# Kernel optimization log

Measured on AMD Instinct MI355X. Metric: run time of the kernel, lower is better.

The kernel has to match this reference:

```python
import jax, jax.numpy as jnp
import numpy as np

STRIDE, PAD, DIL = 1, 1, 1  # from init_kwargs
RELU = True


def setup_inputs() -> dict:
    key = jax.random.key(0)
    k1, k2, k3 = jax.random.split(key, 3)
    B, Cin, Cout, H, W, K = 32, 128, 256, 56, 56, 3
    # uint8 quantized codes stored as float32 (module does .float() before conv)
    x = jnp.round(jax.random.uniform(k1, (B, Cin, H, W), dtype=jnp.float32) * 255.0)
    weight = jnp.round(jax.random.uniform(k2, (Cout, Cin, K, K), dtype=jnp.float32) * 255.0)
    # int32 quantized bias (scale = s_x * s_w, zero_point = 0)
    bias = jnp.round(jax.random.normal(k3, (Cout,), dtype=jnp.float32) * 1000.0)
    return {
        "x": x,
        "weight": weight,
        "bias": bias,
        "M": jnp.float32(0.0021),      # s_x * s_w / s_y
        "x_zero": jnp.float32(128.0),
        "w_zero": jnp.float32(127.0),
        "y_zero": jnp.float32(0.0),
    }


def reference(x, weight, bias, M, x_zero, w_zero, y_zero):
    # x: [B, Cin, H, W] uint8 codes as float; weight: [Cout, Cin, kh, kw]
    xz = x - x_zero                    # zero-point sub (padding adds literal 0s, as in torch: pad AFTER sub)
    w = weight - w_zero
    y = jax.lax.conv_general_dilated(
        xz, w,
        window_strides=(STRIDE, STRIDE),
        padding=((PAD, PAD), (PAD, PAD)),
        rhs_dilation=(DIL, DIL),
        dimension_numbers=("NCHW", "OIHW", "NCHW"),
    )
    y = (y + bias[None, :, None, None]) * M + y_zero  # requantize
    if RELU:
        y = jnp.maximum(y, y_zero)     # clamp below at output zero-point
    return jnp.round(y)
```

## Files before the change

### kernel.cpp

```cpp
#include <hip/hip_runtime.h>
#include <hip/hip_bf16.h>


typedef __attribute__((ext_vector_type(4))) int   i32x4;
typedef __attribute__((ext_vector_type(4))) float f32x4;

#define WTI8_BYTES (18 * 16384)
#define XPI8_BYTES (32 * 58 * 8192)

__device__ __forceinline__ void gload_lds16(const void* g, void* l) {
    __builtin_amdgcn_global_load_lds(
        (const __attribute__((address_space(1))) void*)g,
        (__attribute__((address_space(3))) void*)l, 16, 0, 0);
}

__global__ void wprep_kernel(const float* __restrict__ w, char* __restrict__ wt) {
    int cidx = blockIdx.x * 256 + threadIdx.x;
    int byte0 = cidx * 16;
    int s    = byte0 >> 14;
    int wn   = (byte0 >> 12) & 3;
    int e4   = byte0 & 4095;
    int nn   = e4 >> 6;
    int koff = e4 & 63;
    int kl   = koff ^ ((nn & 3) << 4);
    int n = wn * 64 + nn;
    int r = s >> 1, ch = s & 1;
    union { char c[16]; i32x4 v; } u;
#pragma unroll
    for (int j = 0; j < 16; ++j) {
        int cin = ch * 64 + kl + j;
        u.c[j] = (char)((int)w[(size_t)n * 1152 + cin * 9 + r] - 128);
    }
    *(i32x4*)(wt + byte0) = u.v;
}

__global__ void xprep_kernel(const float* __restrict__ x, const float* __restrict__ xzp,
                             char* __restrict__ xpi8, int* __restrict__ colsum) {
    int bhh = blockIdx.x;
    int b = bhh / 58, hh = bhh % 58;
    int tid = threadIdx.x;
    char* blob = xpi8 + (size_t)bhh * 8192;
    int w  = tid & 63;
    int cq = tid >> 6;
    __shared__ int ps[4][64];
    if (hh == 0 || hh == 57) {
        i32x4 z = {0, 0, 0, 0};
        *(i32x4*)(blob + tid * 32)      = z;
        *(i32x4*)(blob + tid * 32 + 16) = z;
        if (cq == 0) colsum[bhh * 64 + w] = 0;
        return;
    }
    const int ZX = (int)rintf(*xzp);
    bool valid = (w >= 1 && w <= 56);
    const float* xb = x + (size_t)b * 128 * 3136 + (size_t)(hh - 1) * 56 +
                      (valid ? (w - 1) : 0);
    int csum = 0;
#pragma unroll
    for (int u = 0; u < 2; ++u) {
        union { char c[16]; i32x4 v; } uu;
#pragma unroll
        for (int j = 0; j < 16; ++j) {
            int c = cq * 32 + u * 16 + j;
            int val = valid ? ((int)xb[(size_t)c * 3136] - ZX) : 0;
            uu.c[j] = (char)val;
            csum += val;
        }
        *(i32x4*)(blob + w * 128 + ((cq * 32 + u * 16) ^ ((w & 7) << 4))) = uu.v;
    }
    ps[cq][w] = csum;
    __syncthreads();
    if (cq == 0)
        colsum[bhh * 64 + w] = ps[0][w] + ps[1][w] + ps[2][w] + ps[3][w];
}

__global__ __launch_bounds__(256, 2)
void conv_kernel(const char* __restrict__ wt,
                 const char* __restrict__ xpi8,
                 const int* __restrict__ colsum,
                 const float* __restrict__ bias,
                 const float* __restrict__ Mp,
                 const float* __restrict__ wzp,
                 const float* __restrict__ yzp,
                 float* __restrict__ out) {
    __shared__ __align__(1024) char As[32768];
    __shared__ __align__(1024) char Bp[32768];
    __shared__ int s2row[2][64];

    const int tid = threadIdx.x;
    const int lane = tid & 63;
    const int wn = tid >> 6;
    const int l15 = lane & 15, lg = lane >> 4;
    const int bx = blockIdx.x;
    const int b = bx / 28;
    const int h0 = (bx % 28) * 2;

    char* bpriv = Bp + wn * 8192;
    const char* bwsrc = wt + wn * 4096 + lane * 16;
    const int bfoff = (lg * 16) ^ ((l15 & 3) << 4);

    const char* agbase = xpi8 + (size_t)(b * 58 + h0) * 8192;
#pragma unroll
    for (int i = 0; i < 8; ++i)
        gload_lds16(agbase + i * 4096 + tid * 16, As + i * 4096 + tid * 16);
#pragma unroll
    for (int st = 0; st < 2; ++st)
#pragma unroll
        for (int i = 0; i < 4; ++i)
            gload_lds16(bwsrc + (size_t)st * 16384 + i * 1024,
                        bpriv + st * 4096 + i * 1024 + lane * 16);
    if (tid < 128) {
        int row = tid >> 6, m = tid & 63;
        int s = 0;
        if (m < 56) {
#pragma unroll
            for (int kh = 0; kh < 3; ++kh)
#pragma unroll
                for (int kw = 0; kw < 3; ++kw)
                    s += colsum[(b * 58 + h0 + row + kh) * 64 + m + kw];
        }
        s2row[row][m] = s;
    }

    i32x4 acc[4][8];
#pragma unroll
    for (int i = 0; i < 4; ++i)
#pragma unroll
        for (int j = 0; j < 8; ++j)
            acc[i][j] = (i32x4){0, 0, 0, 0};

    __syncthreads();

#pragma unroll
    for (int s = 0; s < 18; ++s) {
        const int kh = (s >> 1) / 3, kw = (s >> 1) % 3, ch = s & 1;
        const char* bslot = bpriv + (s & 1) * 4096;
        i32x4 bfr[4];
#pragma unroll
        for (int fn = 0; fn < 4; ++fn) {
            int nn = fn * 16 + l15;
            bfr[fn] = *(const i32x4*)(bslot + nn * 64 + bfoff);
        }
        i32x4 afr[8];
#pragma unroll
        for (int fm = 0; fm < 8; ++fm) {
            int rowoff = fm >> 2;
            int wv = (fm & 3) * 16 + l15 + kw;
            int wc = wv > 63 ? 63 : wv;
            int ab = (rowoff + kh) * 8192 + wc * 128 +
                     ((ch * 64 + lg * 16) ^ ((wc & 7) << 4));
            afr[fm] = *(const i32x4*)(As + ab);
        }
        if (s < 16) {
            asm volatile("s_waitcnt lgkmcnt(0)" ::: "memory");
#pragma unroll
            for (int i = 0; i < 4; ++i)
                gload_lds16(bwsrc + (size_t)(s + 2) * 16384 + i * 1024,
                            bpriv + (s & 1) * 4096 + i * 1024 + lane * 16);
        }
        if (s < 16)       asm volatile("s_waitcnt vmcnt(4)" ::: "memory");
        else if (s == 16) asm volatile("s_waitcnt vmcnt(0)" ::: "memory");
#pragma unroll
        for (int fn = 0; fn < 4; ++fn)
#pragma unroll
            for (int fm = 0; fm < 8; ++fm)
                acc[fn][fm] = __builtin_amdgcn_mfma_i32_16x16x64_i8(
                    bfr[fn], afr[fm], acc[fn][fm], 0, 0, 0);
    }

    const float Mv  = *Mp;
    const float yzv = *yzp;
    const float CWf = 128.0f - *wzp;
#pragma unroll
    for (int fn = 0; fn < 4; ++fn) {
#pragma unroll
        for (int reg = 0; reg < 4; ++reg) {
            const int cout = wn * 64 + fn * 16 + lg * 4 + reg;
            const float bv = bias[cout];
#pragma unroll
            for (int fm = 0; fm < 8; ++fm) {
                const int row = fm >> 2;
                const int m = (fm & 3) * 16 + l15;
                if (m < 56) {
                    const size_t rowb =
                        ((size_t)(b * 256 + cout) * 56 + h0 + row) * 56;
                    float af = (float)acc[fn][fm][reg] +
                               CWf * (float)s2row[row][m];
                    float v = (af + bv) * Mv + yzv;
                    v = fmaxf(v, yzv);
                    out[rowb + m] = rintf(v);
                }
            }
        }
    }
}

extern "C" void kernel_launch(void* const* d_in, const int* in_sizes, int n_in,
                              void* d_out, int out_size, void* d_ws, size_t ws_size,
                              hipStream_t stream) {
    const float* x    = (const float*)d_in[0];
    const float* w    = (const float*)d_in[1];
    const float* bias = (const float*)d_in[2];
    const float* Mp   = (const float*)d_in[3];
    const float* xzp  = (const float*)d_in[4];
    const float* wzp  = (const float*)d_in[5];
    const float* yzp  = (const float*)d_in[6];
    float* out = (float*)d_out;

    char* wt     = (char*)d_ws;
    char* xpi8   = wt + WTI8_BYTES;
    int*  colsum = (int*)(xpi8 + XPI8_BYTES);

    wprep_kernel<<<72, 256, 0, stream>>>(w, wt);
    xprep_kernel<<<32 * 58, 256, 0, stream>>>(x, xzp, xpi8, colsum);
    conv_kernel<<<32 * 28, 256, 0, stream>>>(wt, xpi8, colsum, bias, Mp, wzp, yzp, out);
}
```

Before: 75.46 us.

## Stage conv epilogue through LDS for vector stores and merge prep kernels

The epilogue now writes requantized outputs into a shared-memory buffer per output row, then stores them to global memory as 16-byte vectors, replacing scattered scalar stores. The weight and activation prep kernels are merged into one launch to save a kernel launch and the gap between launches. The shared allocation grows to about 68 KB, which with the launch bound of 2 blocks per CU may limit occupancy, and the epilogue adds block barriers.

After: 75.20 us. No clear change (-0.3%).

```diff
diff --git a/kernel.cpp b/kernel.cpp
--- a/kernel.cpp
+++ b/kernel.cpp
@@ -14,46 +14,48 @@
         (__attribute__((address_space(3))) void*)l, 16, 0, 0);
 }
 
-__global__ void wprep_kernel(const float* __restrict__ w, char* __restrict__ wt) {
-    int cidx = blockIdx.x * 256 + threadIdx.x;
-    int byte0 = cidx * 16;
-    int s    = byte0 >> 14;
-    int wn   = (byte0 >> 12) & 3;
-    int e4   = byte0 & 4095;
-    int nn   = e4 >> 6;
-    int koff = e4 & 63;
-    int kl   = koff ^ ((nn & 3) << 4);
-    int n = wn * 64 + nn;
-    int r = s >> 1, ch = s & 1;
-    union { char c[16]; i32x4 v; } u;
-#pragma unroll
-    for (int j = 0; j < 16; ++j) {
-        int cin = ch * 64 + kl + j;
-        u.c[j] = (char)((int)w[(size_t)n * 1152 + cin * 9 + r] - 128);
-    }
-    *(i32x4*)(wt + byte0) = u.v;
-}
-
-__global__ void xprep_kernel(const float* __restrict__ x, const float* __restrict__ xzp,
-                             char* __restrict__ xpi8, int* __restrict__ colsum) {
+__global__ void prep_kernel(const float* __restrict__ x, const float* __restrict__ xzp,
+                            const float* __restrict__ w,
+                            char* __restrict__ xpi8, int* __restrict__ colsum,
+                            char* __restrict__ wt) {
+    int tid = threadIdx.x;
+    if (blockIdx.x >= 32 * 58) {
+        int cidx = (blockIdx.x - 32 * 58) * 256 + tid;
+        int byte0 = cidx * 16;
+        int s    = byte0 >> 14;
+        int wn   = (byte0 >> 12) & 3;
+        int e4   = byte0 & 4095;
+        int nn   = e4 >> 6;
+        int koff = e4 & 63;
+        int kl   = koff ^ ((nn & 3) << 4);
+        int n = wn * 64 + nn;
+        int r = s >> 1, ch = s & 1;
+        union { char c[16]; i32x4 v; } u;
+#pragma unroll
+        for (int j = 0; j < 16; ++j) {
+            int cin = ch * 64 + kl + j;
+            u.c[j] = (char)((int)w[(size_t)n * 1152 + cin * 9 + r] - 128);
+        }
+        *(i32x4*)(wt + byte0) = u.v;
+        return;
+    }
     int bhh = blockIdx.x;
     int b = bhh / 58, hh = bhh % 58;
-    int tid = threadIdx.x;
     char* blob = xpi8 + (size_t)bhh * 8192;
-    int w  = tid & 63;
+    int wcol = tid & 63;
     int cq = tid >> 6;
     __shared__ int ps[4][64];
     if (hh == 0 || hh == 57) {
         i32x4 z = {0, 0, 0, 0};
         *(i32x4*)(blob + tid * 32)      = z;
         *(i32x4*)(blob + tid * 32 + 16) = z;
-        if (cq == 0) colsum[bhh * 64 + w] = 0;
+        if (cq == 0) colsum[bhh * 64 + wcol] = 0;
         return;
     }
     const int ZX = (int)rintf(*xzp);
-    bool valid = (w >= 1 && w <= 56);
+    bool valid = (wcol >= 1 && wcol <= 56);
     const float* xb = x + (size_t)b * 128 * 3136 + (size_t)(hh - 1) * 56 +
-                      (valid ? (w - 1) : 0);
+                      (valid ? (wcol - 1) : 0);
     int csum = 0;
 #pragma unroll
     for (int u = 0; u < 2; ++u) {
@@ -65,12 +67,12 @@
             uu.c[j] = (char)val;
             csum += val;
         }
-        *(i32x4*)(blob + w * 128 + ((cq * 32 + u * 16) ^ ((w & 7) << 4))) = uu.v;
-    }
-    ps[cq][w] = csum;
+        *(i32x4*)(blob + wcol * 128 + ((cq * 32 + u * 16) ^ ((wcol & 7) << 4))) = uu.v;
+    }
+    ps[cq][wcol] = csum;
     __syncthreads();
     if (cq == 0)
-        colsum[bhh * 64 + w] = ps[0][w] + ps[1][w] + ps[2][w] + ps[3][w];
+        colsum[bhh * 64 + wcol] = ps[0][wcol] + ps[1][wcol] + ps[2][wcol] + ps[3][wcol];
 }
 
 __global__ __launch_bounds__(256, 2)
@@ -82,9 +84,11 @@
                  const float* __restrict__ wzp,
                  const float* __restrict__ yzp,
                  float* __restrict__ out) {
-    __shared__ __align__(1024) char As[32768];
-    __shared__ __align__(1024) char Bp[32768];
+    __shared__ __align__(1024) char smem[69632];
     __shared__ int s2row[2][64];
+    char* As = smem;
+    char* Bp = smem + 32768;
+    float* fbuf = (float*)smem;
 
     const int tid = threadIdx.x;
     const int lane = tid & 63;
@@ -136,17 +140,14 @@
         const char* bslot = bpriv + (s & 1) * 4096;
         i32x4 bfr[4];
 #pragma unroll
-        for (int fn = 0; fn < 4; ++fn) {
-            int nn = fn * 16 + l15;
-            bfr[fn] = *(const i32x4*)(bslot + nn * 64 + bfoff);
-        }
+        for (int fn = 0; fn < 4; ++fn)
+            bfr[fn] = *(const i32x4*)(bslot + (fn * 16 + l15) * 64 + bfoff);
         i32x4 afr[8];
 #pragma unroll
         for (int fm = 0; fm < 8; ++fm) {
-            int rowoff = fm >> 2;
             int wv = (fm & 3) * 16 + l15 + kw;
             int wc = wv > 63 ? 63 : wv;
-            int ab = (rowoff + kh) * 8192 + wc * 128 +
+            int ab = ((fm >> 2) + kh) * 8192 + wc * 128 +
                      ((ch * 64 + lg * 16) ^ ((wc & 7) << 4));
             afr[fm] = *(const i32x4*)(As + ab);
         }
@@ -156,9 +157,10 @@
             for (int i = 0; i < 4; ++i)
                 gload_lds16(bwsrc + (size_t)(s + 2) * 16384 + i * 1024,
                             bpriv + (s & 1) * 4096 + i * 1024 + lane * 16);
-        }
-        if (s < 16)       asm volatile("s_waitcnt vmcnt(4)" ::: "memory");
-        else if (s == 16) asm volatile("s_waitcnt vmcnt(0)" ::: "memory");
+            asm volatile("s_waitcnt vmcnt(4)" ::: "memory");
+        } else if (s == 16) {
+            asm volatile("s_waitcnt vmcnt(0)" ::: "memory");
+        }
 #pragma unroll
         for (int fn = 0; fn < 4; ++fn)
 #pragma unroll
@@ -171,24 +173,33 @@
     const float yzv = *yzp;
     const float CWf = 128.0f - *wzp;
 #pragma unroll
-    for (int fn = 0; fn < 4; ++fn) {
-#pragma unroll
-        for (int reg = 0; reg < 4; ++reg) {
-            const int cout = wn * 64 + fn * 16 + lg * 4 + reg;
-            const float bv = bias[cout];
-#pragma unroll
-            for (int fm = 0; fm < 8; ++fm) {
-                const int row = fm >> 2;
-                const int m = (fm & 3) * 16 + l15;
-                if (m < 56) {
-                    const size_t rowb =
-                        ((size_t)(b * 256 + cout) * 56 + h0 + row) * 56;
-                    float af = (float)acc[fn][fm][reg] +
+    for (int row = 0; row < 2; ++row) {
+        __syncthreads();
+#pragma unroll
+        for (int fn = 0; fn < 4; ++fn) {
+#pragma unroll
+            for (int reg = 0; reg < 4; ++reg) {
+                const int cout = wn * 64 + fn * 16 + lg * 4 + reg;
+                const float bv = bias[cout];
+#pragma unroll
+                for (int fm4 = 0; fm4 < 4; ++fm4) {
+                    const int m = fm4 * 16 + l15;
+                    float af = (float)acc[fn][row * 4 + fm4][reg] +
                                CWf * (float)s2row[row][m];
-                    float v = (af + bv) * Mv + yzv;
-                    v = fmaxf(v, yzv);
-                    out[rowb + m] = rintf(v);
+                    float v = fmaxf((af + bv) * Mv + yzv, yzv);
+                    fbuf[cout * 66 + m] = rintf(v);
                 }
+            }
+        }
+        __syncthreads();
+        const size_t obase = (size_t)b * 802816 + (size_t)(h0 + row) * 56;
+#pragma unroll
+        for (int k = 0; k < 16; ++k) {
+            int c = tid + k * 256;
+            int cout = c >> 4, m4 = c & 15;
+            if (m4 < 14) {
+                f32x4 vv = *(const f32x4*)&fbuf[cout * 66 + m4 * 4];
+                *(f32x4*)&out[obase + (size_t)cout * 3136 + m4 * 4] = vv;
             }
         }
     }
@@ -210,7 +221,6 @@
     char* xpi8   = wt + WTI8_BYTES;
     int*  colsum = (int*)(xpi8 + XPI8_BYTES);
 
-    wprep_kernel<<<72, 256, 0, stream>>>(w, wt);
-    xprep_kernel<<<32 * 58, 256, 0, stream>>>(x, xzp, xpi8, colsum);
+    prep_kernel<<<32 * 58 + 72, 256, 0, stream>>>(x, xzp, w, xpi8, colsum, wt);
     conv_kernel<<<32 * 28, 256, 0, stream>>>(wt, xpi8, colsum, bias, Mp, wzp, yzp, out);
 }
```
